# Kernel tuning notes

Measured on AMD Instinct MI355X. Metric: run time of the kernel, lower is better.

The kernel has to match this reference:

```python
import jax, jax.numpy as jnp
import numpy as np

LEAKY_SLOPE = 0.01  # torch F.leaky_relu default
LN_EPS = 1e-5       # torch nn.LayerNorm default


def _layer_norm(x, g, b):
    mu = jnp.mean(x, axis=-1, keepdims=True)
    var = jnp.var(x, axis=-1, keepdims=True)
    return (x - mu) * jax.lax.rsqrt(var + LN_EPS) * g + b


def _gcn(x, adj, W, b):
    # GraphConvolution (Kipf-style): adj @ (x @ W) + b
    return adj @ (x @ W) + b


def setup_inputs() -> dict:
    key = jax.random.key(0)
    ks = jax.random.split(key, 8)
    N, fan_in, fan_mid, fan_out = 12288, 128, 128, 20
    h0, h1, h2 = fan_mid, fan_mid // 2, fan_mid // 4  # 128, 64, 32
    inp = {
        "x": jax.random.normal(ks[0], (N, fan_in), dtype=jnp.float32),
        "adj0": jax.random.uniform(ks[1], (N, N), dtype=jnp.float32),
        "adj1": jax.random.uniform(ks[2], (N, N), dtype=jnp.float32),
        "adj2": jax.random.uniform(ks[3], (N, N), dtype=jnp.float32),
        "W0": jax.random.normal(ks[4], (fan_in, h0), dtype=jnp.float32) / np.sqrt(fan_in),
        "b0": jnp.zeros((h0,), dtype=jnp.float32),
        "W1": jax.random.normal(ks[5], (h0, h1), dtype=jnp.float32) / np.sqrt(h0),
        "b1": jnp.zeros((h1,), dtype=jnp.float32),
        "W2": jax.random.normal(ks[6], (h1, h2), dtype=jnp.float32) / np.sqrt(h1),
        "b2": jnp.zeros((h2,), dtype=jnp.float32),
        "g0": jnp.ones((h0,), dtype=jnp.float32),
        "be0": jnp.zeros((h0,), dtype=jnp.float32),
        "g1": jnp.ones((h1,), dtype=jnp.float32),
        "be1": jnp.zeros((h1,), dtype=jnp.float32),
        "g2": jnp.ones((h2,), dtype=jnp.float32),
        "be2": jnp.zeros((h2,), dtype=jnp.float32),
        "Wl": jax.random.normal(ks[7], (h2, fan_out), dtype=jnp.float32) / np.sqrt(h2),
        "bl": jnp.zeros((fan_out,), dtype=jnp.float32),
    }
    return inp


def reference(x, adj0, adj1, adj2, W0, b0, W1, b1, W2, b2,
              g0, be0, g1, be1, g2, be2, Wl, bl):
    # first GCN + LayerNorm (no activation, matching the original forward)
    h = _layer_norm(_gcn(x, adj0, W0, b0), g0, be0)
    # two loop iterations: GCN -> LN -> LeakyReLU -> Dropout(eval=identity)
    h = jax.nn.leaky_relu(_layer_norm(_gcn(h, adj1, W1, b1), g1, be1), LEAKY_SLOPE)
    h = jax.nn.leaky_relu(_layer_norm(_gcn(h, adj2, W2, b2), g2, be2), LEAKY_SLOPE)
    logits = h @ Wl + bl
    return jax.nn.log_softmax(logits, axis=1)
```

## Files before the change

kernel.cpp:

```cpp
#include <hip/hip_runtime.h>
#include <cstdint>
#include <cstddef>

typedef __attribute__((ext_vector_type(8))) short short8;
typedef __attribute__((ext_vector_type(4))) float f32x4;

#define DEV __device__ __forceinline__

DEV unsigned short f2bf(float f) {
  unsigned int u = __float_as_uint(f);
  u += 0x7fffu + ((u >> 16) & 1u);
  return (unsigned short)(u >> 16);
}

DEV unsigned int pk2(float a, float b) {
  return (unsigned int)f2bf(a) | ((unsigned int)f2bf(b) << 16);
}

DEV void glds16(const void* g, void* l) {
  __builtin_amdgcn_global_load_lds(
      (const __attribute__((address_space(1))) void*)g,
      (__attribute__((address_space(3))) void*)l, 16, 0, 0);
}

constexpr int NROW = 12288;

__global__ __launch_bounds__(256) void xw_kernel(
    const float* __restrict__ x, const float* __restrict__ W0,
    unsigned short* __restrict__ t0T) {
  __shared__ float sW[128 * 128];
  __shared__ float sx[16][128];
  const int t = threadIdx.x;
  for (int i = t; i < 128 * 128; i += 256) sW[i] = W0[i];
  const int r0 = blockIdx.x * 16;
  for (int i = t; i < 16 * 128; i += 256)
    sx[i >> 7][i & 127] = x[(size_t)(r0 + (i >> 7)) * 128 + (i & 127)];
  __syncthreads();
  const int c = t & 127;
  const int rg = t >> 7;
  float acc[8] = {0, 0, 0, 0, 0, 0, 0, 0};
  for (int k = 0; k < 128; ++k) {
    float w = sW[k * 128 + c];
#pragma unroll
    for (int j = 0; j < 8; ++j) acc[j] += sx[rg * 8 + j][k] * w;
  }
  uint4 o;
  o.x = pk2(acc[0], acc[1]);
  o.y = pk2(acc[2], acc[3]);
  o.z = pk2(acc[4], acc[5]);
  o.w = pk2(acc[6], acc[7]);
  *(uint4*)(t0T + (size_t)c * NROW + r0 + rg * 8) = o;
}

template <int H>
__global__ __launch_bounds__(256, 3) void gcn_gemm(
    const float* __restrict__ A, const unsigned short* __restrict__ BT,
    float* __restrict__ part) {
  constexpr int KSPLIT = 4;
  constexpr int BM = 64, BK = 64;
  constexpr int NR = H / 16;
  constexpr int NB = H / 32;
  constexpr int KSTEPS = (NROW / KSPLIT) / BK;
  constexpr int BBYTES = H * 128;
  static_assert((KSTEPS & 1) == 0, "");

  __shared__ alignas(16) char ldsB[2 * BBYTES];

  const int t = threadIdx.x;
  const int xcd = blockIdx.x & 7;
  const int idx = blockIdx.x >> 3;
  const int split = xcd >> 1;
  const int bm = ((xcd & 1) ? 96 : 0) + idx;
  const int k0 = split * (NROW / KSPLIT);

  const int wid = t >> 6, lane = t & 63;
  const int l15 = lane & 15, loct = lane >> 4;

  const float* aptr =
      A + (size_t)(bm * BM + wid * 16 + l15) * NROW + k0 + loct * 8;

  const int nB0 = t >> 3;
  const int wB = (t & 7) ^ (nB0 & 7);
  const unsigned short* bptr = BT + (size_t)nB0 * NROW + k0 + wB * 8;
  char* ldsBw = ldsB + wid * 1024;

  int boff[NR][2];
#pragma unroll
  for (int n = 0; n < NR; ++n)
#pragma unroll
    for (int kk = 0; kk < 2; ++kk) {
      int nn = n * 16 + l15;
      boff[n][kk] = (nn * 128 + kk * 64 + loct * 16) ^ ((nn & 7) << 4);
    }

  f32x4 acc[NR];
#pragma unroll
  for (int n = 0; n < NR; ++n) acc[n] = {0.f, 0.f, 0.f, 0.f};

  f32x4 arA[4], arB[4];

  auto issueA = [&](f32x4* ar, int s) {
#pragma unroll
    for (int kk = 0; kk < 2; ++kk)
#pragma unroll
      for (int h = 0; h < 2; ++h)
        ar[kk * 2 + h] = *(const f32x4*)(aptr + s * BK + kk * 32 + h * 4);
  };
  auto glB = [&](int s, int buf) {
#pragma unroll
    for (int j = 0; j < NB; ++j)
      glds16(bptr + (size_t)j * 32 * NROW + s * BK,
             ldsBw + buf * BBYTES + j * 4096);
  };
  auto compute = [&](const f32x4* ar, int buf) {
    const char* lB = ldsB + buf * BBYTES;
#pragma unroll
    for (int kk = 0; kk < 2; ++kk) {
      union { unsigned int u[4]; short8 s8; } afu;
      afu.u[0] = pk2(ar[kk * 2].x, ar[kk * 2].y);
      afu.u[1] = pk2(ar[kk * 2].z, ar[kk * 2].w);
      afu.u[2] = pk2(ar[kk * 2 + 1].x, ar[kk * 2 + 1].y);
      afu.u[3] = pk2(ar[kk * 2 + 1].z, ar[kk * 2 + 1].w);
      const short8 af = afu.s8;
#pragma unroll
      for (int n = 0; n < NR; ++n) {
        const short8 bf = *(const short8*)(lB + boff[n][kk]);
        acc[n] = __builtin_amdgcn_mfma_f32_16x16x32_bf16(af, bf, acc[n],
                                                         0, 0, 0);
      }
    }
  };

  glB(0, 0);
  __builtin_amdgcn_sched_barrier(0);
  issueA(arA, 0);
  issueA(arB, 1);
  asm volatile("s_waitcnt vmcnt(4)" ::: "memory");
  __builtin_amdgcn_s_barrier();
  __builtin_amdgcn_sched_barrier(0);

  for (int s = 0; s < KSTEPS - 2; s += 2) {
    glB(s + 1, 1);
    __builtin_amdgcn_sched_barrier(0);
    compute(arA, 0);
    issueA(arA, s + 2);
    asm volatile("s_waitcnt vmcnt(4) lgkmcnt(0)" ::: "memory");
    __builtin_amdgcn_s_barrier();
    __builtin_amdgcn_sched_barrier(0);
    glB(s + 2, 0);
    __builtin_amdgcn_sched_barrier(0);
    compute(arB, 1);
    issueA(arB, s + 3);
    asm volatile("s_waitcnt vmcnt(4) lgkmcnt(0)" ::: "memory");
    __builtin_amdgcn_s_barrier();
    __builtin_amdgcn_sched_barrier(0);
  }

  glB(KSTEPS - 1, 1);
  __builtin_amdgcn_sched_barrier(0);
  compute(arA, 0);
  asm volatile("s_waitcnt vmcnt(0) lgkmcnt(0)" ::: "memory");
  __builtin_amdgcn_s_barrier();
  __builtin_amdgcn_sched_barrier(0);
  compute(arB, 1);

  float* pout = part + ((size_t)split * NROW + (size_t)bm * BM + wid * 16) * H;
#pragma unroll
  for (int n = 0; n < NR; ++n)
#pragma unroll
    for (int rr = 0; rr < 4; ++rr)
      pout[(size_t)(loct * 4 + rr) * H + n * 16 + l15] = acc[n][rr];
}

template <int H, int H2, bool ACT>
__global__ __launch_bounds__(256) void reduce_ln(
    const float* __restrict__ part, const float* __restrict__ bias,
    const float* __restrict__ g, const float* __restrict__ be,
    const float* __restrict__ Wn, unsigned short* __restrict__ tT) {
  __shared__ float sW[H * H2];
  __shared__ float sh[4][H];
  const int t = threadIdx.x;
  for (int i = t; i < H * H2; i += 256) sW[i] = Wn[i];
  __syncthreads();

  const int wid = t >> 6, lane = t & 63;
  const int row = blockIdx.x * 4 + wid;
  constexpr int CPL = H / 64;
  float v[CPL];
#pragma unroll
  for (int c = 0; c < CPL; ++c) {
    const int col = lane + c * 64;
    float s = bias[col];
#pragma unroll
    for (int sp = 0; sp < 4; ++sp)
      s += part[((size_t)sp * NROW + row) * H + col];
    v[c] = s;
  }
  float sum = 0;
#pragma unroll
  for (int c = 0; c < CPL; ++c) sum += v[c];
#pragma unroll
  for (int o = 32; o > 0; o >>= 1) sum += __shfl_xor(sum, o);
  const float mu = sum / H;
  float vs = 0;
#pragma unroll
  for (int c = 0; c < CPL; ++c) { float d = v[c] - mu; vs += d * d; }
#pragma unroll
  for (int o = 32; o > 0; o >>= 1) vs += __shfl_xor(vs, o);
  const float rstd = rsqrtf(vs / H + 1e-5f);
#pragma unroll
  for (int c = 0; c < CPL; ++c) {
    const int col = lane + c * 64;
    float h = (v[c] - mu) * rstd * g[col] + be[col];
    if (ACT) h = (h > 0.f) ? h : 0.01f * h;
    sh[wid][col] = h;
  }
  __syncthreads();
  if (lane < H2) {
    float d = 0;
#pragma unroll 8
    for (int k = 0; k < H; ++k) d += sh[wid][k] * sW[k * H2 + lane];
    tT[(size_t)lane * NROW + row] = f2bf(d);
  }
}

__global__ __launch_bounds__(256) void reduce_final(
    const float* __restrict__ part, const float* __restrict__ bias,
    const float* __restrict__ g, const float* __restrict__ be,
    const float* __restrict__ Wl, const float* __restrict__ bl,
    float* __restrict__ out) {
  __shared__ float sW[32 * 20];
  __shared__ float sbl[20];
  __shared__ float sh[4][32];
  __shared__ float sl[4][20];
  const int t = threadIdx.x;
  for (int i = t; i < 640; i += 256) sW[i] = Wl[i];
  if (t < 20) sbl[t] = bl[t];
  __syncthreads();
  const int wid = t >> 6, lane = t & 63;
  const int row = blockIdx.x * 4 + wid;
  const int col = lane & 31;
  float v = bias[col];
#pragma unroll
  for (int sp = 0; sp < 4; ++sp)
    v += part[((size_t)sp * NROW + row) * 32 + col];
  float sum = v;
#pragma unroll
  for (int o = 32; o > 0; o >>= 1) sum += __shfl_xor(sum, o);
  const float mu = sum / 64.f;
  float d0 = v - mu;
  float vs = d0 * d0;
#pragma unroll
  for (int o = 32; o > 0; o >>= 1) vs += __shfl_xor(vs, o);
  const float rstd = rsqrtf(vs / 64.f + 1e-5f);
  float h = (v - mu) * rstd * g[col] + be[col];
  h = (h > 0.f) ? h : 0.01f * h;
  if (lane < 32) sh[wid][col] = h;
  __syncthreads();
  if (lane < 20) {
    float lg = sbl[lane];
#pragma unroll
    for (int k = 0; k < 32; ++k) lg += sh[wid][k] * sW[k * 20 + lane];
    sl[wid][lane] = lg;
  }
  __syncthreads();
  if (lane < 20) {
    float mx = -1e30f;
#pragma unroll
    for (int k = 0; k < 20; ++k) mx = fmaxf(mx, sl[wid][k]);
    float se = 0.f;
#pragma unroll
    for (int k = 0; k < 20; ++k) se += expf(sl[wid][k] - mx);
    out[(size_t)row * 20 + lane] = sl[wid][lane] - mx - logf(se);
  }
}

extern "C" void kernel_launch(void* const* d_in, const int* in_sizes, int n_in,
                              void* d_out, int out_size, void* d_ws,
                              size_t ws_size, hipStream_t stream) {
  const float* x    = (const float*)d_in[0];
  const float* adj0 = (const float*)d_in[1];
  const float* adj1 = (const float*)d_in[2];
  const float* adj2 = (const float*)d_in[3];
  const float* W0   = (const float*)d_in[4];
  const float* b0   = (const float*)d_in[5];
  const float* W1   = (const float*)d_in[6];
  const float* b1   = (const float*)d_in[7];
  const float* W2   = (const float*)d_in[8];
  const float* b2   = (const float*)d_in[9];
  const float* g0   = (const float*)d_in[10];
  const float* be0  = (const float*)d_in[11];
  const float* g1   = (const float*)d_in[12];
  const float* be1  = (const float*)d_in[13];
  const float* g2   = (const float*)d_in[14];
  const float* be2  = (const float*)d_in[15];
  const float* Wl   = (const float*)d_in[16];
  const float* bl   = (const float*)d_in[17];
  float* out = (float*)d_out;

  char* ws = (char*)d_ws;
  float* part =          (float*)(ws);
  unsigned short* t0T = (unsigned short*)(ws + 25165824);
  unsigned short* t1T = (unsigned short*)(ws + 25165824 + 3145728);
  unsigned short* t2T = (unsigned short*)(ws + 25165824 + 3145728 + 1572864);

  xw_kernel<<<NROW / 16, 256, 0, stream>>>(x, W0, t0T);
  gcn_gemm<128><<<(NROW / 64) * 4, 256, 0, stream>>>(adj0, t0T, part);
  reduce_ln<128, 64, false><<<NROW / 4, 256, 0, stream>>>(part, b0, g0, be0, W1, t1T);
  gcn_gemm<64><<<(NROW / 64) * 4, 256, 0, stream>>>(adj1, t1T, part);
  reduce_ln<64, 32, true><<<NROW / 4, 256, 0, stream>>>(part, b1, g1, be1, W2, t2T);
  gcn_gemm<32><<<(NROW / 64) * 4, 256, 0, stream>>>(adj2, t2T, part);
  reduce_final<<<NROW / 4, 256, 0, stream>>>(part, b2, g2, be2, Wl, bl, out);
}
```

Baseline: 481.3 us.

## Stage A tiles through LDS with superstep prefetch and halve the K-split

```diff
diff --git a/kernel.cpp b/kernel.cpp
--- a/kernel.cpp
+++ b/kernel.cpp
@@ -56,40 +56,48 @@
 __global__ __launch_bounds__(256, 3) void gcn_gemm(
     const float* __restrict__ A, const unsigned short* __restrict__ BT,
     float* __restrict__ part) {
-  constexpr int KSPLIT = 4;
-  constexpr int BM = 64, BK = 64;
-  constexpr int NR = H / 16;
+  constexpr int BM = 32, BK = 64;
+  constexpr int NR = H / 32;
   constexpr int NB = H / 32;
-  constexpr int KSTEPS = (NROW / KSPLIT) / BK;
+  constexpr int KHALF = NROW / 2;
+  constexpr int KSTEPS = KHALF / BK;
+  constexpr int NSUP = KSTEPS / 6;
   constexpr int BBYTES = H * 128;
-  static_assert((KSTEPS & 1) == 0, "");
-
+
+  __shared__ alignas(16) char ldsA[2 * 4096];
   __shared__ alignas(16) char ldsB[2 * BBYTES];
 
   const int t = threadIdx.x;
   const int xcd = blockIdx.x & 7;
   const int idx = blockIdx.x >> 3;
-  const int split = xcd >> 1;
-  const int bm = ((xcd & 1) ? 96 : 0) + idx;
-  const int k0 = split * (NROW / KSPLIT);
-
-  const int wid = t >> 6, lane = t & 63;
-  const int l15 = lane & 15, loct = lane >> 4;
-
-  const float* aptr =
-      A + (size_t)(bm * BM + wid * 16 + l15) * NROW + k0 + loct * 8;
+  const int split = xcd >> 2;
+  const int bm = (xcd & 3) * 96 + idx;
+  const int k0 = split * KHALF;
+
+  const int r = t >> 3, q = t & 7;
+  const float* aptr = A + (size_t)(bm * BM + r) * NROW + k0 + q * 8;
+  const int aw = (r * 128 + q * 16) ^ ((r & 7) << 4);
 
   const int nB0 = t >> 3;
   const int wB = (t & 7) ^ (nB0 & 7);
   const unsigned short* bptr = BT + (size_t)nB0 * NROW + k0 + wB * 8;
+  const int wid = t >> 6;
   char* ldsBw = ldsB + wid * 1024;
 
-  int boff[NR][2];
+  const int lane = t & 63;
+  const int l15 = lane & 15, loct = lane >> 4;
+  const int wm = wid >> 1, wn = wid & 1;
+  int aoff[2], boff[NR][2];
+#pragma unroll
+  for (int kk = 0; kk < 2; ++kk) {
+    const int row = wm * 16 + l15;
+    aoff[kk] = (row * 128 + kk * 64 + loct * 16) ^ ((row & 7) << 4);
+  }
 #pragma unroll
   for (int n = 0; n < NR; ++n)
 #pragma unroll
     for (int kk = 0; kk < 2; ++kk) {
-      int nn = n * 16 + l15;
+      const int nn = wn * (NR * 16) + n * 16 + l15;
       boff[n][kk] = (nn * 128 + kk * 64 + loct * 16) ^ ((nn & 7) << 4);
     }
 
@@ -97,14 +105,14 @@
 #pragma unroll
   for (int n = 0; n < NR; ++n) acc[n] = {0.f, 0.f, 0.f, 0.f};
 
-  f32x4 arA[4], arB[4];
-
-  auto issueA = [&](f32x4* ar, int s) {
-#pragma unroll
-    for (int kk = 0; kk < 2; ++kk)
-#pragma unroll
-      for (int h = 0; h < 2; ++h)
-        ar[kk * 2 + h] = *(const f32x4*)(aptr + s * BK + kk * 32 + h * 4);
+  f32x4 av[12];
+
+  auto issueSuper = [&](int S) {
+#pragma unroll
+    for (int j = 0; j < 6; ++j) {
+      av[2 * j]     = *(const f32x4*)(aptr + S * 384 + j * 64);
+      av[2 * j + 1] = *(const f32x4*)(aptr + S * 384 + j * 64 + 4);
+    }
   };
   auto glB = [&](int s, int buf) {
 #pragma unroll
@@ -112,16 +120,20 @@
       glds16(bptr + (size_t)j * 32 * NROW + s * BK,
              ldsBw + buf * BBYTES + j * 4096);
   };
-  auto compute = [&](const f32x4* ar, int buf) {
+  auto cvtWrite = [&](int j, int buf) {
+    uint4 w;
+    w.x = pk2(av[2 * j].x, av[2 * j].y);
+    w.y = pk2(av[2 * j].z, av[2 * j].w);
+    w.z = pk2(av[2 * j + 1].x, av[2 * j + 1].y);
+    w.w = pk2(av[2 * j + 1].z, av[2 * j + 1].w);
+    *(uint4*)(ldsA + buf * 4096 + aw) = w;
+  };
+  auto compute = [&](int buf) {
+    const char* lA = ldsA + buf * 4096;
     const char* lB = ldsB + buf * BBYTES;
 #pragma unroll
     for (int kk = 0; kk < 2; ++kk) {
-      union { unsigned int u[4]; short8 s8; } afu;
-      afu.u[0] = pk2(ar[kk * 2].x, ar[kk * 2].y);
-      afu.u[1] = pk2(ar[kk * 2].z, ar[kk * 2].w);
-      afu.u[2] = pk2(ar[kk * 2 + 1].x, ar[kk * 2 + 1].y);
-      afu.u[3] = pk2(ar[kk * 2 + 1].z, ar[kk * 2 + 1].w);
-      const short8 af = afu.s8;
+      const short8 af = *(const short8*)(lA + aoff[kk]);
 #pragma unroll
       for (int n = 0; n < NR; ++n) {
         const short8 bf = *(const short8*)(lB + boff[n][kk]);
@@ -131,45 +143,67 @@
     }
   };
 
+#define WAITBAR(vmstr)                                        \
+  asm volatile("s_waitcnt " vmstr " lgkmcnt(0)" ::: "memory"); \
+  __builtin_amdgcn_s_barrier();                                \
+  __builtin_amdgcn_sched_barrier(0);
+
   glB(0, 0);
   __builtin_amdgcn_sched_barrier(0);
-  issueA(arA, 0);
-  issueA(arB, 1);
-  asm volatile("s_waitcnt vmcnt(4)" ::: "memory");
-  __builtin_amdgcn_s_barrier();
-  __builtin_amdgcn_sched_barrier(0);
-
-  for (int s = 0; s < KSTEPS - 2; s += 2) {
+  issueSuper(0);
+  asm volatile("s_waitcnt vmcnt(12)" ::: "memory");
+  cvtWrite(0, 0);
+  WAITBAR("vmcnt(12)");
+
+  for (int S = 0; S < NSUP - 1; ++S) {
+    const int s = 6 * S;
     glB(s + 1, 1);
+    compute(0);
+    cvtWrite(1, 1);
+    WAITBAR("vmcnt(0)");
+    glB(s + 2, 0);
+    compute(1);
+    cvtWrite(2, 0);
+    WAITBAR("vmcnt(0)");
+    glB(s + 3, 1);
+    compute(0);
+    cvtWrite(3, 1);
+    WAITBAR("vmcnt(0)");
+    glB(s + 4, 0);
+    compute(1);
+    cvtWrite(4, 0);
+    WAITBAR("vmcnt(0)");
+    glB(s + 5, 1);
     __builtin_amdgcn_sched_barrier(0);
-    compute(arA, 0);
-    issueA(arA, s + 2);
-    asm volatile("s_waitcnt vmcnt(4) lgkmcnt(0)" ::: "memory");
-    __builtin_amdgcn_s_barrier();
-    __builtin_amdgcn_sched_barrier(0);
-    glB(s + 2, 0);
-    __builtin_amdgcn_sched_barrier(0);
-    compute(arB, 1);
-    issueA(arB, s + 3);
-    asm volatile("s_waitcnt vmcnt(4) lgkmcnt(0)" ::: "memory");
-    __builtin_amdgcn_s_barrier();
-    __builtin_amdgcn_sched_barrier(0);
-  }
-
-  glB(KSTEPS - 1, 1);
-  __builtin_amdgcn_sched_barrier(0);
-  compute(arA, 0);
-  asm volatile("s_waitcnt vmcnt(0) lgkmcnt(0)" ::: "memory");
-  __builtin_amdgcn_s_barrier();
-  __builtin_amdgcn_sched_barrier(0);
-  compute(arB, 1);
-
-  float* pout = part + ((size_t)split * NROW + (size_t)bm * BM + wid * 16) * H;
+    compute(0);
+    cvtWrite(5, 1);
+    issueSuper(S + 1);
+    WAITBAR("vmcnt(12)");
+    glB(s + 6, 0);
+    compute(1);
+    cvtWrite(0, 0);
+    WAITBAR("vmcnt(0)");
+  }
+
+  {
+    const int s = 6 * (NSUP - 1);
+    glB(s + 1, 1); compute(0); cvtWrite(1, 1); WAITBAR("vmcnt(0)");
+    glB(s + 2, 0); compute(1); cvtWrite(2, 0); WAITBAR("vmcnt(0)");
+    glB(s + 3, 1); compute(0); cvtWrite(3, 1); WAITBAR("vmcnt(0)");
+    glB(s + 4, 0); compute(1); cvtWrite(4, 0); WAITBAR("vmcnt(0)");
+    glB(s + 5, 1); compute(0); cvtWrite(5, 1); WAITBAR("vmcnt(0)");
+    compute(1);
+  }
+#undef WAITBAR
+
+  float* pout =
+      part + ((size_t)split * NROW + (size_t)bm * BM + wm * 16) * H;
 #pragma unroll
   for (int n = 0; n < NR; ++n)
 #pragma unroll
     for (int rr = 0; rr < 4; ++rr)
-      pout[(size_t)(loct * 4 + rr) * H + n * 16 + l15] = acc[n][rr];
+      pout[(size_t)(loct * 4 + rr) * H + wn * (NR * 16) + n * 16 + l15] =
+          acc[n][rr];
 }
 
 template <int H, int H2, bool ACT>
@@ -192,7 +226,7 @@
     const int col = lane + c * 64;
     float s = bias[col];
 #pragma unroll
-    for (int sp = 0; sp < 4; ++sp)
+    for (int sp = 0; sp < 2; ++sp)
       s += part[((size_t)sp * NROW + row) * H + col];
     v[c] = s;
   }
@@ -242,7 +276,7 @@
   const int col = lane & 31;
   float v = bias[col];
 #pragma unroll
-  for (int sp = 0; sp < 4; ++sp)
+  for (int sp = 0; sp < 2; ++sp)
     v += part[((size_t)sp * NROW + row) * 32 + col];
   float sum = v;
 #pragma unroll
@@ -305,10 +339,10 @@
   unsigned short* t2T = (unsigned short*)(ws + 25165824 + 3145728 + 1572864);
 
   xw_kernel<<<NROW / 16, 256, 0, stream>>>(x, W0, t0T);
-  gcn_gemm<128><<<(NROW / 64) * 4, 256, 0, stream>>>(adj0, t0T, part);
+  gcn_gemm<128><<<768, 256, 0, stream>>>(adj0, t0T, part);
   reduce_ln<128, 64, false><<<NROW / 4, 256, 0, stream>>>(part, b0, g0, be0, W1, t1T);
-  gcn_gemm<64><<<(NROW / 64) * 4, 256, 0, stream>>>(adj1, t1T, part);
+  gcn_gemm<64><<<768, 256, 0, stream>>>(adj1, t1T, part);
   reduce_ln<64, 32, true><<<NROW / 4, 256, 0, stream>>>(part, b1, g1, be1, W2, t2T);
-  gcn_gemm<32><<<(NROW / 64) * 4, 256, 0, stream>>>(adj2, t2T, part);
+  gcn_gemm<32><<<768, 256, 0, stream>>>(adj2, t2T, part);
   reduce_final<<<NROW / 4, 256, 0, stream>>>(part, b2, g2, be2, Wl, bl, out);
 }
```

After: 468.1 us. 2.8% less time.
